# Kernel tuning notes

Hardware: AMD Instinct MI355X
Metric: run time of the kernel (lower is better)

## Reference

```python
import jax, jax.numpy as jnp
import numpy as np

B, NV, FD = 16, 128, 8192
T_TEMP = 0.2      # self.T
MARGIN = 1.0      # nn.TripletMarginLoss default
EPS = 1e-6        # pairwise_distance eps


def _l2norm(x):
    # torch F.normalize(dim=1): x / max(||x||, 1e-12)
    nrm = jnp.maximum(jnp.linalg.norm(x, axis=-1, keepdims=True), 1e-12)
    return x / nrm


def _ssl_parts(qb, kb, nb, num_gt):
    # qb,kb,nb: [NV, FD] flattened reid embeddings for one image
    qv = _l2norm(qb)[:num_gt]          # [g, FD]
    kv = _l2norm(kb)[:num_gt]          # [g, FD]
    nv = _l2norm(nb)                   # [NV, FD] (negatives are NOT sliced)
    g = num_gt
    S = qv @ kv.T                      # [g, g] all pairwise dots (replaces torch.dot loops)
    # similarity-matrix loss
    sm = jnp.sum((S - jnp.eye(g, dtype=S.dtype)) ** 2) / (g * g)
    # pairwise distances with torch eps convention: ||a - b + eps||_2
    # = sqrt(||a||^2 + ||b||^2 - 2 a.b + 2*eps*(sum(a)-sum(b)) + D*eps^2); ||a||=||b||=1
    sq = qv.sum(axis=1)                # [g]
    sk = kv.sum(axis=1)                # [g]
    const = FD * EPS * EPS
    d_qk = jnp.sqrt(jnp.maximum(2.0 - 2.0 * S + 2.0 * EPS * (sq[:, None] - sk[None, :]) + const, 0.0))
    d_kq = jnp.sqrt(jnp.maximum(2.0 - 2.0 * S.T + 2.0 * EPS * (sk[:, None] - sq[None, :]) + const, 0.0))
    off = 1.0 - jnp.eye(g, dtype=S.dtype)
    # triplet: anc=q_i,pos=k_i,neg=k_j  and  anc=k_i,pos=q_i,neg=q_j, j != i
    tri1 = jnp.sum(jax.nn.relu(jnp.diag(d_qk)[:, None] - d_qk + MARGIN) * off)
    tri2 = jnp.sum(jax.nn.relu(jnp.diag(d_kq)[:, None] - d_kq + MARGIN) * off)
    tri_sum = tri1 + tri2
    # cycle consistency: |q_i.k_j - k_i.q_j| = |S[i,j] - S[j,i]|
    cyc = jnp.sum(jnp.abs(S - S.T) * off) / (g * (g - 1))
    # InfoNCE: l_pos = q_i.k_i, l_neg = q @ n.T
    l_pos = jnp.diag(S)[:, None]       # [g, 1]
    l_neg = qv @ nv.T                  # [g, NV]
    logits = jnp.concatenate([l_pos, l_neg], axis=1) / T_TEMP
    ce = jnp.mean(jax.nn.logsumexp(logits, axis=1) - logits[:, 0])  # CE with labels=0
    return sm, tri_sum, cyc, ce / g


def setup_inputs() -> dict:
    key = jax.random.key(0)
    kq, kk, kn = jax.random.split(key, 3)
    q = jax.random.normal(kq, (B, NV, FD), dtype=jnp.float32)
    k = jax.random.normal(kk, (B, NV, FD), dtype=jnp.float32)
    n = jax.random.normal(kn, (B, NV, FD), dtype=jnp.float32)
    return {"q": q, "k": k, "n": n, "num_gt": NV}


def reference(q, k, n, num_gt):
    sm, tri, cyc, ce = jax.vmap(lambda a, b, c: _ssl_parts(a, b, c, num_gt))(q, k, n)
    tri_cnt = 2 * num_gt * (num_gt - 1)
    # original bug: tri_loss accumulates across batches while tri_cnt resets,
    # so each batch contributes cumsum(tri)[b] / tri_cnt
    ssl = jnp.sum(sm) + jnp.sum(jnp.cumsum(tri)) / tri_cnt + jnp.sum(cyc) + jnp.sum(ce)
    return ssl
```

## Files before the change

kernel.cpp:

```cpp
#include <hip/hip_runtime.h>
#include <cstdint>
#include <cstddef>

#define B_N   16
#define G_N   128
#define FD_N  8192
#define BK    64

typedef unsigned short u16;
typedef u16  u16x4 __attribute__((ext_vector_type(4)));
typedef u16  u16x8 __attribute__((ext_vector_type(8)));
typedef __bf16 bf16x8 __attribute__((ext_vector_type(8)));
typedef float f32x16 __attribute__((ext_vector_type(16)));

#define STATS_SSQ_Q 0
#define STATS_SUM_Q 2048
#define STATS_SSQ_K 4096
#define STATS_SUM_K 6144
#define STATS_SSQ_N 8192
#define STATS_FLOATS 10240
#define RES_OFF   10240
#define CRED_OFF  10304
#define PART_OFF  534592

__device__ __forceinline__ u16 f2bf(float f) {
    uint32_t u = __float_as_uint(f);
    u += 0x7FFFu + ((u >> 16) & 1u);
    return (u16)(u >> 16);
}

__global__ __launch_bounds__(512, 2)
void k_gemm(const float* __restrict__ q, const float* __restrict__ kM,
            const float* __restrict__ nM, float* __restrict__ ws,
            int ksplit, int kc)
{
    __shared__ __align__(16) u16 sA[G_N * BK];
    __shared__ __align__(16) u16 sB[2 * G_N * BK];

    const int tid = threadIdx.x;
    const int blk = blockIdx.x;
    const int b   = blk / ksplit;
    const int kch = blk - b * ksplit;
    const int niter = kc / BK;

    const size_t mat_off = (size_t)b * G_N * FD_N + (size_t)kch * kc + (size_t)(tid & 15) * 4;
    const float* qp = q  + mat_off;
    const float* kp = kM + mat_off;
    const float* np = nM + mat_off;
    const int r0 = tid >> 4;
    const int c4 = tid & 15;

    float4 la[4], lb[8];
    float aS[4] = {0.f,0.f,0.f,0.f}, aQ[4] = {0.f,0.f,0.f,0.f};
    float bS[8] = {0.f,0.f,0.f,0.f,0.f,0.f,0.f,0.f};
    float bQ[8] = {0.f,0.f,0.f,0.f,0.f,0.f,0.f,0.f};

    #pragma unroll
    for (int i = 0; i < 4; ++i) la[i]   = *(const float4*)(qp + (size_t)(r0 + 32*i) * FD_N);
    #pragma unroll
    for (int i = 0; i < 4; ++i) lb[i]   = *(const float4*)(kp + (size_t)(r0 + 32*i) * FD_N);
    #pragma unroll
    for (int i = 0; i < 4; ++i) lb[4+i] = *(const float4*)(np + (size_t)(r0 + 32*i) * FD_N);

    const int lane  = tid & 63;
    const int wv    = tid >> 6;
    const int wm    = wv >> 2;
    const int wn    = wv & 3;
    const int khalf = lane >> 5;
    const int lrow  = lane & 31;

    f32x16 acc[2][2];
    #pragma unroll
    for (int mb = 0; mb < 2; ++mb)
      #pragma unroll
      for (int nb = 0; nb < 2; ++nb)
        #pragma unroll
        for (int e = 0; e < 16; ++e) acc[mb][nb][e] = 0.f;

    int wA[4], wB[8];
    #pragma unroll
    for (int i = 0; i < 4; ++i) { int row = r0 + 32*i; wA[i] = row*BK + (((c4>>1) ^ (row&7))<<3) + ((c4&1)<<2); }
    #pragma unroll
    for (int i = 0; i < 8; ++i) { int row = r0 + 32*i; wB[i] = row*BK + (((c4>>1) ^ (row&7))<<3) + ((c4&1)<<2); }

    const int rA0 = wm*64 + lrow;
    const int rB0 = wn*64 + lrow;

    for (int kb = 0; kb < niter; ++kb) {
        __syncthreads();
        #pragma unroll
        for (int i = 0; i < 4; ++i) {
            float4 v = la[i];
            aS[i] += v.x + v.y + v.z + v.w;
            aQ[i] += v.x*v.x + v.y*v.y + v.z*v.z + v.w*v.w;
            u16x4 h; h[0]=f2bf(v.x); h[1]=f2bf(v.y); h[2]=f2bf(v.z); h[3]=f2bf(v.w);
            *(u16x4*)(sA + wA[i]) = h;
        }
        #pragma unroll
        for (int i = 0; i < 8; ++i) {
            float4 v = lb[i];
            bS[i] += v.x + v.y + v.z + v.w;
            bQ[i] += v.x*v.x + v.y*v.y + v.z*v.z + v.w*v.w;
            u16x4 h; h[0]=f2bf(v.x); h[1]=f2bf(v.y); h[2]=f2bf(v.z); h[3]=f2bf(v.w);
            *(u16x4*)(sB + wB[i]) = h;
        }
        __syncthreads();
        if (kb + 1 < niter) {
            const float* qn = qp + (kb+1)*BK;
            const float* kn = kp + (kb+1)*BK;
            const float* nn = np + (kb+1)*BK;
            #pragma unroll
            for (int i = 0; i < 4; ++i) la[i]   = *(const float4*)(qn + (size_t)(r0 + 32*i) * FD_N);
            #pragma unroll
            for (int i = 0; i < 4; ++i) lb[i]   = *(const float4*)(kn + (size_t)(r0 + 32*i) * FD_N);
            #pragma unroll
            for (int i = 0; i < 4; ++i) lb[4+i] = *(const float4*)(nn + (size_t)(r0 + 32*i) * FD_N);
        }
        #pragma unroll
        for (int s = 0; s < 4; ++s) {
            int chunk = s*2 + khalf;
            bf16x8 af[2], bf[2];
            #pragma unroll
            for (int mb = 0; mb < 2; ++mb) {
                int row = rA0 + mb*32;
                u16x8 raw = *(const u16x8*)(sA + row*BK + (((chunk) ^ (row&7))<<3));
                af[mb] = __builtin_bit_cast(bf16x8, raw);
            }
            #pragma unroll
            for (int nb = 0; nb < 2; ++nb) {
                int row = rB0 + nb*32;
                u16x8 raw = *(const u16x8*)(sB + row*BK + (((chunk) ^ (row&7))<<3));
                bf[nb] = __builtin_bit_cast(bf16x8, raw);
            }
            #pragma unroll
            for (int mb = 0; mb < 2; ++mb)
              #pragma unroll
              for (int nb = 0; nb < 2; ++nb)
                acc[mb][nb] = __builtin_amdgcn_mfma_f32_32x32x16_bf16(af[mb], bf[nb], acc[mb][nb], 0, 0, 0);
        }
    }

    float* part = ws + PART_OFF + (size_t)blk * (G_N * 256);
    #pragma unroll
    for (int mb = 0; mb < 2; ++mb)
      #pragma unroll
      for (int nb = 0; nb < 2; ++nb) {
        int col = wn*64 + nb*32 + lrow;
        int rbase = wm*64 + mb*32 + 4*khalf;
        #pragma unroll
        for (int reg = 0; reg < 16; ++reg) {
            int row = rbase + (reg & 3) + 8*(reg >> 2);
            part[(size_t)row * 256 + col] = acc[mb][nb][reg];
        }
      }

    #pragma unroll
    for (int i = 0; i < 4; ++i) {
        float s = aS[i], qq = aQ[i];
        for (int m = 8; m >= 1; m >>= 1) { s += __shfl_xor(s, m, 64); qq += __shfl_xor(qq, m, 64); }
        if ((lane & 15) == 0) {
            int row = r0 + 32*i;
            atomicAdd(ws + STATS_SUM_Q + b*G_N + row, s);
            atomicAdd(ws + STATS_SSQ_Q + b*G_N + row, qq);
        }
    }
    #pragma unroll
    for (int i = 0; i < 8; ++i) {
        float s = bS[i], qq = bQ[i];
        for (int m = 8; m >= 1; m >>= 1) { s += __shfl_xor(s, m, 64); qq += __shfl_xor(qq, m, 64); }
        if ((lane & 15) == 0) {
            int row = r0 + 32*i;
            if (row < G_N) {
                atomicAdd(ws + STATS_SUM_K + b*G_N + row, s);
                atomicAdd(ws + STATS_SSQ_K + b*G_N + row, qq);
            } else {
                atomicAdd(ws + STATS_SSQ_N + b*G_N + (row - G_N), qq);
            }
        }
    }
}

__global__ void k_red(float* __restrict__ ws, int ksplit)
{
    int idx = blockIdx.x * 256 + threadIdx.x;
    int b = idx >> 15;
    int w = idx & 32767;
    const float* p = ws + PART_OFF + ((size_t)(b * ksplit) << 15);
    float s = 0.f;
    for (int ksi = 0; ksi < ksplit; ++ksi) s += p[((size_t)ksi << 15) + w];
    ws[CRED_OFF + idx] = s;
}

__global__ __launch_bounds__(256)
void k_epi(float* __restrict__ ws)
{
    const int b = blockIdx.x;
    const int t = threadIdx.x;
    __shared__ float invq[128], invk[128], invn[128], sqv[128], skv[128], ddq[128], ddk[128];
    __shared__ float rbuf[4][4];

    const float c0 = (float)FD_N * 1e-6f * 1e-6f;

    if (t < 128) {
        float iq = 1.f / fmaxf(sqrtf(ws[STATS_SSQ_Q + b*128 + t]), 1e-12f);
        invq[t] = iq;
        sqv[t]  = ws[STATS_SUM_Q + b*128 + t] * iq;
        float ik = 1.f / fmaxf(sqrtf(ws[STATS_SSQ_K + b*128 + t]), 1e-12f);
        invk[t] = ik;
        skv[t]  = ws[STATS_SUM_K + b*128 + t] * ik;
        invn[t] = 1.f / fmaxf(sqrtf(ws[STATS_SSQ_N + b*128 + t]), 1e-12f);
    }
    __syncthreads();
    const float* C = ws + CRED_OFF + (size_t)b * 32768;
    if (t < 128) {
        float S_ii = C[t*256 + t] * invq[t] * invk[t];
        ddq[t] = sqrtf(fmaxf(2.f - 2.f*S_ii + 2e-6f*(sqv[t]-skv[t]) + c0, 0.f));
        ddk[t] = sqrtf(fmaxf(2.f - 2.f*S_ii + 2e-6f*(skv[t]-sqv[t]) + c0, 0.f));
    }
    __syncthreads();

    float sm = 0.f, tri = 0.f, cyc = 0.f, ce = 0.f;
    for (int idx = t; idx < 16384; idx += 256) {
        int i = idx >> 7, j = idx & 127;
        float S_ij = C[i*256 + j] * invq[i] * invk[j];
        float dd = S_ij - (i == j ? 1.f : 0.f);
        sm += dd * dd;
        if (i != j) {
            float dqk = sqrtf(fmaxf(2.f - 2.f*S_ij + 2e-6f*(sqv[i]-skv[j]) + c0, 0.f));
            tri += fmaxf(ddq[i] - dqk + 1.f, 0.f);
            float dkq = sqrtf(fmaxf(2.f - 2.f*S_ij + 2e-6f*(skv[j]-sqv[i]) + c0, 0.f));
            tri += fmaxf(ddk[j] - dkq + 1.f, 0.f);
            float S_ji = C[j*256 + i] * invq[j] * invk[i];
            cyc += fabsf(S_ij - S_ji);
        }
    }
    if (t < 128) {
        float iq = invq[t];
        float lp = C[t*256 + t] * iq * invk[t] * 5.0f;
        float ssum = __expf(lp);
        for (int j = 0; j < 128; ++j) {
            float ln = C[t*256 + 128 + j] * iq * invn[j] * 5.0f;
            ssum += __expf(ln);
        }
        ce = __logf(ssum) - lp;
    }

    for (int m = 32; m >= 1; m >>= 1) {
        sm  += __shfl_xor(sm,  m, 64);
        tri += __shfl_xor(tri, m, 64);
        cyc += __shfl_xor(cyc, m, 64);
        ce  += __shfl_xor(ce,  m, 64);
    }
    int wvi = t >> 6, ln0 = t & 63;
    if (ln0 == 0) { rbuf[wvi][0] = sm; rbuf[wvi][1] = tri; rbuf[wvi][2] = cyc; rbuf[wvi][3] = ce; }
    __syncthreads();
    if (t == 0) {
        float SM = 0, TR = 0, CY = 0, CE = 0;
        for (int w2 = 0; w2 < 4; ++w2) { SM += rbuf[w2][0]; TR += rbuf[w2][1]; CY += rbuf[w2][2]; CE += rbuf[w2][3]; }
        float* r = ws + RES_OFF + b*4;
        r[0] = SM / 16384.f;
        r[1] = TR;
        r[2] = CY / (128.f * 127.f);
        r[3] = CE / 16384.f;
    }
}

__global__ void k_fin(const float* __restrict__ ws, float* __restrict__ out)
{
    int l = threadIdx.x;
    float v = 0.f;
    if (l < 16) {
        const float* r = ws + RES_OFF + l*4;
        v = r[0] + r[2] + r[3] + (float)(16 - l) * r[1] / 32512.f;
    }
    for (int m = 8; m >= 1; m >>= 1) v += __shfl_xor(v, m, 64);
    if (l == 0) out[0] = v;
}

extern "C" void kernel_launch(void* const* d_in, const int* in_sizes, int n_in,
                              void* d_out, int out_size, void* d_ws, size_t ws_size,
                              hipStream_t stream)
{
    const float* q  = (const float*)d_in[0];
    const float* kM = (const float*)d_in[1];
    const float* nM = (const float*)d_in[2];
    float* ws  = (float*)d_ws;
    float* out = (float*)d_out;

    int ksplit = 16;
    while (ksplit > 1 &&
           ((size_t)PART_OFF + (size_t)ksplit * B_N * 32768) * sizeof(float) > ws_size)
        ksplit >>= 1;
    int kc = FD_N / ksplit;

    hipMemsetAsync(d_ws, 0, STATS_FLOATS * sizeof(float), stream);
    k_gemm<<<B_N * ksplit, 512, 0, stream>>>(q, kM, nM, ws, ksplit, kc);
    k_red<<<(B_N * 32768) / 256, 256, 0, stream>>>(ws, ksplit);
    k_epi<<<B_N, 256, 0, stream>>>(ws);
    k_fin<<<1, 64, 0, stream>>>(ws, out);
}
```

Measured before the change: 258.9 us.

## Raise split-K and occupancy, vectorize reduction, stage S in LDS, fuse final reduce

```diff
diff --git a/kernel.cpp b/kernel.cpp
--- a/kernel.cpp
+++ b/kernel.cpp
@@ -19,9 +19,8 @@
 #define STATS_SUM_K 6144
 #define STATS_SSQ_N 8192
 #define STATS_FLOATS 10240
-#define RES_OFF   10240
-#define CRED_OFF  10304
-#define PART_OFF  534592
+#define CRED_OFF  10240
+#define PART_OFF  534528
 
 __device__ __forceinline__ u16 f2bf(float f) {
     uint32_t u = __float_as_uint(f);
@@ -29,7 +28,9 @@
     return (u16)(u >> 16);
 }
 
-__global__ __launch_bounds__(512, 2)
+#define LDS_BARRIER() asm volatile("s_waitcnt lgkmcnt(0)\n\ts_barrier" ::: "memory")
+
+__global__ __launch_bounds__(512, 4)
 void k_gemm(const float* __restrict__ q, const float* __restrict__ kM,
             const float* __restrict__ nM, float* __restrict__ ws,
             int ksplit, int kc)
@@ -87,7 +88,7 @@
     const int rB0 = wn*64 + lrow;
 
     for (int kb = 0; kb < niter; ++kb) {
-        __syncthreads();
+        LDS_BARRIER();
         #pragma unroll
         for (int i = 0; i < 4; ++i) {
             float4 v = la[i];
@@ -104,7 +105,7 @@
             u16x4 h; h[0]=f2bf(v.x); h[1]=f2bf(v.y); h[2]=f2bf(v.z); h[3]=f2bf(v.w);
             *(u16x4*)(sB + wB[i]) = h;
         }
-        __syncthreads();
+        LDS_BARRIER();
         if (kb + 1 < niter) {
             const float* qn = qp + (kb+1)*BK;
             const float* kn = kp + (kb+1)*BK;
@@ -180,24 +181,29 @@
     }
 }
 
-__global__ void k_red(float* __restrict__ ws, int ksplit)
+__global__ __launch_bounds__(256)
+void k_red(float* __restrict__ ws, int ksplit)
 {
     int idx = blockIdx.x * 256 + threadIdx.x;
-    int b = idx >> 15;
-    int w = idx & 32767;
-    const float* p = ws + PART_OFF + ((size_t)(b * ksplit) << 15);
-    float s = 0.f;
-    for (int ksi = 0; ksi < ksplit; ++ksi) s += p[((size_t)ksi << 15) + w];
-    ws[CRED_OFF + idx] = s;
+    int b = idx >> 13;
+    int w = idx & 8191;
+    const float4* p = (const float4*)(ws + PART_OFF) + (size_t)b * ksplit * 8192 + w;
+    float4 s = {0.f, 0.f, 0.f, 0.f};
+    for (int ksi = 0; ksi < ksplit; ++ksi) {
+        float4 v = p[(size_t)ksi * 8192];
+        s.x += v.x; s.y += v.y; s.z += v.z; s.w += v.w;
+    }
+    ((float4*)(ws + CRED_OFF))[idx] = s;
 }
 
 __global__ __launch_bounds__(256)
-void k_epi(float* __restrict__ ws)
+void k_epi(float* __restrict__ ws, float* __restrict__ out)
 {
     const int b = blockIdx.x;
     const int t = threadIdx.x;
     __shared__ float invq[128], invk[128], invn[128], sqv[128], skv[128], ddq[128], ddk[128];
-    __shared__ float rbuf[4][4];
+    __shared__ float sS[128 * 129];
+    __shared__ float rbuf[4];
 
     const float c0 = (float)FD_N * 1e-6f * 1e-6f;
 
@@ -212,8 +218,13 @@
     }
     __syncthreads();
     const float* C = ws + CRED_OFF + (size_t)b * 32768;
+    for (int idx = t; idx < 16384; idx += 256) {
+        int i = idx >> 7, j = idx & 127;
+        sS[i*129 + j] = C[i*256 + j] * invq[i] * invk[j];
+    }
+    __syncthreads();
     if (t < 128) {
-        float S_ii = C[t*256 + t] * invq[t] * invk[t];
+        float S_ii = sS[t*129 + t];
         ddq[t] = sqrtf(fmaxf(2.f - 2.f*S_ii + 2e-6f*(sqv[t]-skv[t]) + c0, 0.f));
         ddk[t] = sqrtf(fmaxf(2.f - 2.f*S_ii + 2e-6f*(skv[t]-sqv[t]) + c0, 0.f));
     }
@@ -222,7 +233,7 @@
     float sm = 0.f, tri = 0.f, cyc = 0.f, ce = 0.f;
     for (int idx = t; idx < 16384; idx += 256) {
         int i = idx >> 7, j = idx & 127;
-        float S_ij = C[i*256 + j] * invq[i] * invk[j];
+        float S_ij = sS[i*129 + j];
         float dd = S_ij - (i == j ? 1.f : 0.f);
         sm += dd * dd;
         if (i != j) {
@@ -230,13 +241,12 @@
             tri += fmaxf(ddq[i] - dqk + 1.f, 0.f);
             float dkq = sqrtf(fmaxf(2.f - 2.f*S_ij + 2e-6f*(skv[j]-sqv[i]) + c0, 0.f));
             tri += fmaxf(ddk[j] - dkq + 1.f, 0.f);
-            float S_ji = C[j*256 + i] * invq[j] * invk[i];
-            cyc += fabsf(S_ij - S_ji);
+            cyc += fabsf(S_ij - sS[j*129 + i]);
         }
     }
     if (t < 128) {
         float iq = invq[t];
-        float lp = C[t*256 + t] * iq * invk[t] * 5.0f;
+        float lp = sS[t*129 + t] * 5.0f;
         float ssum = __expf(lp);
         for (int j = 0; j < 128; ++j) {
             float ln = C[t*256 + 128 + j] * iq * invn[j] * 5.0f;
@@ -245,36 +255,13 @@
         ce = __logf(ssum) - lp;
     }
 
-    for (int m = 32; m >= 1; m >>= 1) {
-        sm  += __shfl_xor(sm,  m, 64);
-        tri += __shfl_xor(tri, m, 64);
-        cyc += __shfl_xor(cyc, m, 64);
-        ce  += __shfl_xor(ce,  m, 64);
-    }
+    float contrib = sm / 16384.f + cyc / 16256.f + ce / 16384.f
+                  + (float)(16 - b) * tri / 32512.f;
+    for (int m = 32; m >= 1; m >>= 1) contrib += __shfl_xor(contrib, m, 64);
     int wvi = t >> 6, ln0 = t & 63;
-    if (ln0 == 0) { rbuf[wvi][0] = sm; rbuf[wvi][1] = tri; rbuf[wvi][2] = cyc; rbuf[wvi][3] = ce; }
-    __syncthreads();
-    if (t == 0) {
-        float SM = 0, TR = 0, CY = 0, CE = 0;
-        for (int w2 = 0; w2 < 4; ++w2) { SM += rbuf[w2][0]; TR += rbuf[w2][1]; CY += rbuf[w2][2]; CE += rbuf[w2][3]; }
-        float* r = ws + RES_OFF + b*4;
-        r[0] = SM / 16384.f;
-        r[1] = TR;
-        r[2] = CY / (128.f * 127.f);
-        r[3] = CE / 16384.f;
-    }
-}
-
-__global__ void k_fin(const float* __restrict__ ws, float* __restrict__ out)
-{
-    int l = threadIdx.x;
-    float v = 0.f;
-    if (l < 16) {
-        const float* r = ws + RES_OFF + l*4;
-        v = r[0] + r[2] + r[3] + (float)(16 - l) * r[1] / 32512.f;
-    }
-    for (int m = 8; m >= 1; m >>= 1) v += __shfl_xor(v, m, 64);
-    if (l == 0) out[0] = v;
+    if (ln0 == 0) rbuf[wvi] = contrib;
+    __syncthreads();
+    if (t == 0) atomicAdd(out, rbuf[0] + rbuf[1] + rbuf[2] + rbuf[3]);
 }
 
 extern "C" void kernel_launch(void* const* d_in, const int* in_sizes, int n_in,
@@ -287,15 +274,15 @@
     float* ws  = (float*)d_ws;
     float* out = (float*)d_out;
 
-    int ksplit = 16;
+    int ksplit = 32;
     while (ksplit > 1 &&
            ((size_t)PART_OFF + (size_t)ksplit * B_N * 32768) * sizeof(float) > ws_size)
         ksplit >>= 1;
     int kc = FD_N / ksplit;
 
     hipMemsetAsync(d_ws, 0, STATS_FLOATS * sizeof(float), stream);
+    hipMemsetAsync(d_out, 0, sizeof(float), stream);
     k_gemm<<<B_N * ksplit, 512, 0, stream>>>(q, kM, nM, ws, ksplit, kc);
-    k_red<<<(B_N * 32768) / 256, 256, 0, stream>>>(ws, ksplit);
-    k_epi<<<B_N, 256, 0, stream>>>(ws);
-    k_fin<<<1, 64, 0, stream>>>(ws, out);
-}
+    k_red<<<(B_N * 32768 / 4) / 256, 256, 0, stream>>>(ws, ksplit);
+    k_epi<<<B_N, 256, 0, stream>>>(ws, out);
+}
```

Result: slower. 335.0 us (+29.4%).
